# Optimization experiments

Hardware: AMD Instinct MI355X
Metric: run time of the kernel (lower is better)

Reference implementation:

```python
import jax, jax.numpy as jnp
import numpy as np

B, L, D, H = 2, 2048, 512, 8
DH = D // H
THRESHOLD = 0.1


def setup_inputs() -> dict:
    key = jax.random.key(0)
    ks = jax.random.split(key, 8)
    s = 0.02  # weight scale to keep activations sane
    return {
        "q_x": jax.random.normal(ks[0], (B, L, D), jnp.float32),
        "k_x": jax.random.normal(ks[1], (B, L, D), jnp.float32),
        "v_x": jax.random.normal(ks[2], (B, L, D), jnp.float32),
        "energy_coeffs": jax.random.normal(ks[3], (B, L, 16), jnp.float32),
        "Wq": jax.random.normal(ks[4], (D, D), jnp.float32) * s,
        "bq": jnp.zeros((D,), jnp.float32),
        "Wk": jax.random.normal(ks[5], (D, D), jnp.float32) * s,
        "bk": jnp.zeros((D,), jnp.float32),
        "Wv": jax.random.normal(ks[6], (D, D), jnp.float32) * s,
        "bv": jnp.zeros((D,), jnp.float32),
        "Wo": jax.random.normal(ks[7], (D, D), jnp.float32) * s,
        "bo": jnp.zeros((D,), jnp.float32),
    }


def reference(q_x, k_x, v_x, energy_coeffs, Wq, bq, Wk, bk, Wv, bv, Wo, bo):
    b, l, d = q_x.shape
    # QKV projections (torch Linear: x @ W.T + b), split heads -> [B,H,L,Dh]
    Q = (q_x @ Wq.T + bq).reshape(b, l, H, DH).transpose(0, 2, 1, 3)
    K = (k_x @ Wk.T + bk).reshape(b, -1, H, DH).transpose(0, 2, 1, 3)
    V = (v_x @ Wv.T + bv).reshape(b, -1, H, DH).transpose(0, 2, 1, 3)
    scores = jnp.einsum("bhqd,bhkd->bhqk", Q, K) / jnp.sqrt(jnp.float32(DH))
    # straight-through energy-based key mask
    energy = jnp.abs(energy_coeffs).mean(axis=-1)  # [B, Lk]
    soft = jax.nn.sigmoid((energy - THRESHOLD) * 10.0)
    hard = (energy > THRESHOLD).astype(q_x.dtype)
    mask_val = soft + jax.lax.stop_gradient(hard - soft)  # fwd=hard, grad=soft
    scores = scores + (1.0 - mask_val)[:, None, None, :] * (-1e9)
    attn = jax.nn.softmax(scores, axis=-1)
    out = jnp.einsum("bhqk,bhkd->bhqd", attn, V)
    out = out.transpose(0, 2, 1, 3).reshape(b, l, d)
    return out @ Wo.T + bo
```

## Files before the change

### kernel.cpp

```cpp
#include <hip/hip_runtime.h>
#include <stdint.h>

#define B_ 2
#define L_ 2048
#define D_ 512
#define H_ 8
#define DH_ 64

using frag8 = __attribute__((ext_vector_type(8))) short;
using bf4   = __attribute__((ext_vector_type(4))) short;
using f32x4 = __attribute__((ext_vector_type(4))) float;
using u32x4 = __attribute__((ext_vector_type(4))) unsigned int;

#define QSC 0.18033688011112042f

__device__ __forceinline__ unsigned short f2bf(float f) {
    unsigned int u = __float_as_uint(f);
    u += 0x7fffu + ((u >> 16) & 1u);
    return (unsigned short)(u >> 16);
}

__device__ __forceinline__ unsigned int cvtpk(float lo, float hi_) {
    unsigned int r;
    asm("v_cvt_pk_bf16_f32 %0, %1, %2" : "=v"(r) : "v"(lo), "v"(hi_));
    return r;
}

__device__ __forceinline__ void gl2lds16(const void* g, void* lds) {
    __builtin_amdgcn_global_load_lds((const __attribute__((address_space(1))) void*)g,
                                     (__attribute__((address_space(3))) void*)lds,
                                     16, 0, 0);
}

template<int N>
__device__ __forceinline__ void vmwait() {
    asm volatile("s_waitcnt vmcnt(%0)" :: "n"(N) : "memory");
}

__global__ __launch_bounds__(256) void cvt_mask_kernel(
    const float* __restrict__ qx, const float* __restrict__ kx, const float* __restrict__ vx,
    const float* __restrict__ Wq, const float* __restrict__ Wk, const float* __restrict__ Wv,
    const float* __restrict__ Wo, const float* __restrict__ ec,
    unsigned short* qb, unsigned short* kb, unsigned short* vb,
    unsigned short* wqb, unsigned short* wkb, unsigned short* wvb, unsigned short* wob,
    float* __restrict__ mk)
{
    const long NA = (long)B_ * L_ * D_;
    const long NW = (long)D_ * D_;
    const long total4 = (3 * NA + 4 * NW) / 4;
    long q4 = (long)blockIdx.x * 256 + threadIdx.x;
    if (q4 < total4) {
        long i = q4 * 4;
        const float* src; unsigned short* dst; long off;
        if (i < NA)            { src = qx; dst = qb; off = i; }
        else if (i < 2 * NA)   { src = kx; dst = kb; off = i - NA; }
        else if (i < 3 * NA)   { src = vx; dst = vb; off = i - 2 * NA; }
        else {
            long j = i - 3 * NA;
            int w = (int)(j / NW);
            off = j - (long)w * NW;
            src = (w == 0) ? Wq : (w == 1) ? Wk : (w == 2) ? Wv : Wo;
            dst = (w == 0) ? wqb : (w == 1) ? wkb : (w == 2) ? wvb : wob;
        }
        float4 v = *(const float4*)(src + off);
        ushort4 o;
        o.x = f2bf(v.x); o.y = f2bf(v.y); o.z = f2bf(v.z); o.w = f2bf(v.w);
        *(ushort4*)(dst + off) = o;
    } else {
        long i = q4 - total4;
        if (i < B_ * L_) {
            const float4* p4 = (const float4*)(ec + i * 16);
            float s = 0.0f;
#pragma unroll
            for (int j = 0; j < 4; ++j) {
                float4 v = p4[j];
                s += fabsf(v.x) + fabsf(v.y) + fabsf(v.z) + fabsf(v.w);
            }
            float energy = s * (1.0f / 16.0f);
            mk[i] = (energy > 0.1f) ? 0.0f : -1.0e9f;
        }
    }
}

struct GemmArgs { const unsigned short* A; const unsigned short* W;
                  const float* bias; void* C; int mode; };

template<int BM, int BN>
__global__ __launch_bounds__(256) void gemm_kernel(GemmArgs a0, GemmArgs a1, GemmArgs a2,
                                                   int M, int N, int K)
{
    const int nwg = gridDim.x * gridDim.y * gridDim.z;
    int flat = blockIdx.x + gridDim.x * (blockIdx.y + gridDim.y * blockIdx.z);
    int swz  = (flat & 7) * (nwg >> 3) + (flat >> 3);
    const int bx = swz % gridDim.x;
    int t2 = swz / gridDim.x;
    const int by = t2 % gridDim.y;
    const int bz = t2 / gridDim.y;

    GemmArgs ga = bz == 0 ? a0 : (bz == 1 ? a1 : a2);
    const unsigned short* __restrict__ A = ga.A;
    const unsigned short* __restrict__ W = ga.W;
    const float* __restrict__ bias = ga.bias;

    constexpr int MF = BM / 32;
    constexpr int NF = BN / 32;
    constexpr int NL = BM / 32 + BN / 32;

    __shared__ __align__(16) unsigned short As[2][BM * 64];
    __shared__ __align__(16) unsigned short Bs[2][BN * 64];

    const int tid  = threadIdx.x;
    const int lane = tid & 63;
    const int wave = tid >> 6;
    const int hi   = lane >> 4;
    const int ln   = lane & 15;
    const int wr   = wave >> 1;
    const int wc   = wave & 1;

    const long mBase = (long)by * BM;
    const long nBase = (long)bx * BN;

    f32x4 acc[MF][NF];
#pragma unroll
    for (int m = 0; m < MF; ++m)
#pragma unroll
        for (int n = 0; n < NF; ++n) acc[m][n] = (f32x4){0.f, 0.f, 0.f, 0.f};

#define GSTAGE(KT, BUF) do {                                                    \
    _Pragma("unroll")                                                           \
    for (int i_ = 0; i_ < BM / 32; ++i_) {                                      \
        int cl_ = i_ * 256 + tid;                                               \
        int r_ = cl_ >> 3, c_ = cl_ & 7, s_ = c_ ^ (r_ & 7);                    \
        gl2lds16(A + (mBase + r_) * K + (KT) + s_ * 8, As[BUF] + cl_ * 8);      \
    }                                                                           \
    _Pragma("unroll")                                                           \
    for (int i_ = 0; i_ < BN / 32; ++i_) {                                      \
        int cl_ = i_ * 256 + tid;                                               \
        int r_ = cl_ >> 3, c_ = cl_ & 7, s_ = c_ ^ (r_ & 7);                    \
        gl2lds16(W + (nBase + r_) * K + (KT) + s_ * 8, Bs[BUF] + cl_ * 8);      \
    }                                                                           \
} while (0)

    GSTAGE(0, 0);

    const int nk = K / 64;
    for (int t = 0; t < nk; ++t) {
        const int buf = t & 1;
        if (t + 1 < nk) {
            GSTAGE((t + 1) * 64, buf ^ 1);
            vmwait<NL>();
        } else {
            vmwait<0>();
        }
        __builtin_amdgcn_s_barrier();
        __builtin_amdgcn_sched_barrier(0);

        frag8 af[2][MF], bfr[2][NF];
#pragma unroll
        for (int kk = 0; kk < 2; ++kk) {
#pragma unroll
            for (int m = 0; m < MF; ++m) {
                int row = wr * (BM / 2) + m * 16 + ln;
                int c = (kk * 4 + hi) ^ (row & 7);
                af[kk][m] = *(const frag8*)(As[buf] + row * 64 + c * 8);
            }
#pragma unroll
            for (int n = 0; n < NF; ++n) {
                int row = wc * (BN / 2) + n * 16 + ln;
                int c = (kk * 4 + hi) ^ (row & 7);
                bfr[kk][n] = *(const frag8*)(Bs[buf] + row * 64 + c * 8);
            }
        }
        __builtin_amdgcn_s_setprio(1);
#pragma unroll
        for (int kk = 0; kk < 2; ++kk)
#pragma unroll
            for (int m = 0; m < MF; ++m)
#pragma unroll
                for (int n = 0; n < NF; ++n)
                    acc[m][n] = __builtin_amdgcn_mfma_f32_16x16x32_bf16(af[kk][m], bfr[kk][n], acc[m][n], 0, 0, 0);
        __builtin_amdgcn_s_setprio(0);
        __builtin_amdgcn_sched_barrier(0);
        __builtin_amdgcn_s_barrier();
    }
#undef GSTAGE

    const int mode = ga.mode;
#pragma unroll
    for (int m = 0; m < MF; ++m) {
#pragma unroll
        for (int n = 0; n < NF; ++n) {
            long col = nBase + wc * (BN / 2) + n * 16 + ln;
            float bv = bias[col];
#pragma unroll
            for (int j = 0; j < 4; ++j) {
                long row = mBase + wr * (BM / 2) + m * 16 + hi * 4 + j;
                float v = acc[m][n][j] + bv;
                if (mode == 3) {
                    ((float*)ga.C)[row * N + col] = v;
                } else if (mode == 2) {
                    int dh = (int)col & 63;
                    int swv = ((dh & 7) << 1) | ((dh >> 3) & 1);
                    long nt = (row & ~63L) | (long)(((((int)(row >> 2)) & 15) ^ swv) << 2) | (row & 3);
                    ((unsigned short*)ga.C)[col * (long)(B_ * L_) + nt] = f2bf(v);
                } else {
                    if (mode == 1) v *= QSC;
                    ((unsigned short*)ga.C)[row * N + col] = f2bf(v);
                }
            }
        }
    }
}

__global__ __launch_bounds__(512, 4) void attn_kernel(
    const unsigned short* __restrict__ Qg, const unsigned short* __restrict__ Kg,
    const unsigned short* __restrict__ Vt, const float* __restrict__ mkg,
    unsigned short* __restrict__ Og)
{
    const int tid  = threadIdx.x;
    const int lane = tid & 63;
    const int wave = tid >> 6;
    const int grp  = wave >> 2;
    const int wq   = wave & 3;
    const int gtid = tid & 255;
    const int hi   = lane >> 4;
    const int ln   = lane & 15;

    const int bh = blockIdx.y;
    const int b  = bh >> 3, h = bh & 7;
    const unsigned short* Qb = Qg + ((long)b * L_) * D_ + h * DH_;
    const unsigned short* Kb = Kg + ((long)b * L_) * D_ + h * DH_;
    const unsigned short* Vb = Vt + (long)(h * DH_) * (B_ * L_) + (long)b * L_;
    const float* mkb = mkg + (long)b * L_;

    __shared__ __align__(16) char smem[65536];
    unsigned short* KsG = (unsigned short*)(smem + grp * 32768);
    unsigned short* VsG = (unsigned short*)(smem + grp * 32768 + 16384);

    const int q0 = blockIdx.x * 64 + wq * 16;

    frag8 qf[2];
#pragma unroll
    for (int ks = 0; ks < 2; ++ks)
        qf[ks] = *(const frag8*)(Qb + (long)(q0 + ln) * D_ + ks * 32 + hi * 8);

    const int sw  = ((ln & 7) << 1) | ((ln >> 3) & 1);
    const int sl0 = ((hi     ) ^ sw) << 2;
    const int sl1 = ((hi + 4 ) ^ sw) << 2;
    const int sl2 = ((hi + 8 ) ^ sw) << 2;
    const int sl3 = ((hi + 12) ^ sw) << 2;

#define STAGE(TT, BUF) do {                                                     \
    _Pragma("unroll")                                                           \
    for (int c2_ = 0; c2_ < 2; ++c2_) {                                         \
        int cl_ = c2_ * 256 + gtid;                                             \
        int r_ = cl_ >> 3, c_ = cl_ & 7;                                        \
        gl2lds16(Kb + (long)((TT) * 64 + r_) * D_ + ((c_ ^ (r_ & 7)) << 3),     \
                 KsG + (BUF) * 4096 + cl_ * 8);                                 \
        gl2lds16(Vb + (long)r_ * (B_ * L_) + (TT) * 64 + (c_ << 3),             \
                 VsG + (BUF) * 4096 + cl_ * 8);                                 \
    }                                                                           \
} while (0)

    f32x4 o[4];
#pragma unroll
    for (int g = 0; g < 4; ++g) o[g] = (f32x4){0.f, 0.f, 0.f, 0.f};
    float m_run = -__builtin_inff();
    float l_run = 0.0f;
    float scp[16];

    auto SOFTPV = [&](const unsigned short* Vl) {
        float a0 = fmaxf(fmaxf(scp[0], scp[1]), scp[2]);
        float a1 = fmaxf(fmaxf(scp[3], scp[4]), scp[5]);
        float a2 = fmaxf(fmaxf(scp[6], scp[7]), scp[8]);
        float a3 = fmaxf(fmaxf(scp[9], scp[10]), scp[11]);
        float a4 = fmaxf(fmaxf(scp[12], scp[13]), scp[14]);
        float tl = fmaxf(fmaxf(fmaxf(a0, a1), a2), fmaxf(fmaxf(a3, a4), scp[15]));
        float tmax = fmaxf(tl, __shfl_xor(tl, 16));
        tmax = fmaxf(tmax, __shfl_xor(tmax, 32));

        if (!__all(tmax <= m_run + 8.0f)) {
            float m_new = fmaxf(m_run, tmax);
            float alpha = __builtin_amdgcn_exp2f(m_run - m_new);
            float b0 = __shfl(alpha, 4 * hi + 0);
            float b1 = __shfl(alpha, 4 * hi + 1);
            float b2 = __shfl(alpha, 4 * hi + 2);
            float b3 = __shfl(alpha, 4 * hi + 3);
#pragma unroll
            for (int g = 0; g < 4; ++g) {
                o[g][0] *= b0; o[g][1] *= b1; o[g][2] *= b2; o[g][3] *= b3;
            }
            l_run *= alpha;
            m_run = m_new;
        }

        float p[16];
#pragma unroll
        for (int j = 0; j < 16; ++j) p[j] = __builtin_amdgcn_exp2f(scp[j] - m_run);
        float s01 = (p[0] + p[1]) + (p[2] + p[3]);
        float s23 = (p[4] + p[5]) + (p[6] + p[7]);
        float s45 = (p[8] + p[9]) + (p[10] + p[11]);
        float s67 = (p[12] + p[13]) + (p[14] + p[15]);
        float ps = (s01 + s23) + (s45 + s67);
        ps += __shfl_xor(ps, 16);
        ps += __shfl_xor(ps, 32);
        l_run += ps;

        union PU { u32x4 u; frag8 f; } p0u, p1u;
        p0u.u = (u32x4){cvtpk(p[0], p[1]),  cvtpk(p[2], p[3]),
                        cvtpk(p[4], p[5]),  cvtpk(p[6], p[7])};
        p1u.u = (u32x4){cvtpk(p[8], p[9]),  cvtpk(p[10], p[11]),
                        cvtpk(p[12], p[13]), cvtpk(p[14], p[15])};

        __builtin_amdgcn_s_setprio(1);
#pragma unroll
        for (int g = 0; g < 4; ++g) {
            int rowb = (g * 16 + ln) * 64;
            bf4 v0 = *(const bf4*)(Vl + rowb + sl0);
            bf4 v1 = *(const bf4*)(Vl + rowb + sl1);
            bf4 v2 = *(const bf4*)(Vl + rowb + sl2);
            bf4 v3 = *(const bf4*)(Vl + rowb + sl3);
            frag8 vf0 = __builtin_shufflevector(v0, v1, 0, 1, 2, 3, 4, 5, 6, 7);
            frag8 vf1 = __builtin_shufflevector(v2, v3, 0, 1, 2, 3, 4, 5, 6, 7);
            o[g] = __builtin_amdgcn_mfma_f32_16x16x32_bf16(p0u.f, vf0, o[g], 0, 0, 0);
            o[g] = __builtin_amdgcn_mfma_f32_16x16x32_bf16(p1u.f, vf1, o[g], 0, 0, 0);
        }
        __builtin_amdgcn_s_setprio(0);
    };

    auto QKSAVE = [&](const unsigned short* Kl, int T) {
        float4 m40 = *(const float4*)(mkb + T * 64 +      4 * hi);
        float4 m41 = *(const float4*)(mkb + T * 64 + 16 + 4 * hi);
        float4 m42 = *(const float4*)(mkb + T * 64 + 32 + 4 * hi);
        float4 m43 = *(const float4*)(mkb + T * 64 + 48 + 4 * hi);
        f32x4 sv[4];
#pragma unroll
        for (int sh = 0; sh < 4; ++sh) sv[sh] = (f32x4){0.f, 0.f, 0.f, 0.f};
        __builtin_amdgcn_s_setprio(1);
#pragma unroll
        for (int sh = 0; sh < 4; ++sh) {
            int key = sh * 16 + ln;
#pragma unroll
            for (int ks = 0; ks < 2; ++ks) {
                frag8 kf = *(const frag8*)(Kl + key * 64 + (((ks * 4 + hi) ^ (ln & 7)) << 3));
                sv[sh] = __builtin_amdgcn_mfma_f32_16x16x32_bf16(kf, qf[ks], sv[sh], 0, 0, 0);
            }
        }
        __builtin_amdgcn_s_setprio(0);
        scp[0]  = sv[0][0] + m40.x; scp[1]  = sv[0][1] + m40.y;
        scp[2]  = sv[0][2] + m40.z; scp[3]  = sv[0][3] + m40.w;
        scp[4]  = sv[1][0] + m41.x; scp[5]  = sv[1][1] + m41.y;
        scp[6]  = sv[1][2] + m41.z; scp[7]  = sv[1][3] + m41.w;
        scp[8]  = sv[2][0] + m42.x; scp[9]  = sv[2][1] + m42.y;
        scp[10] = sv[2][2] + m42.z; scp[11] = sv[2][3] + m42.w;
        scp[12] = sv[3][0] + m43.x; scp[13] = sv[3][1] + m43.y;
        scp[14] = sv[3][2] + m43.z; scp[15] = sv[3][3] + m43.w;
    };

    STAGE(grp, 0);
    vmwait<0>();
    __builtin_amdgcn_s_barrier();
    __builtin_amdgcn_sched_barrier(0);
    STAGE(2 + grp, 1);
    QKSAVE(KsG, grp);

    for (int i = 1; i < 16; ++i) {
        const int buf = i & 1;
        SOFTPV(VsG + (buf ^ 1) * 4096);
        vmwait<0>();
        __builtin_amdgcn_s_barrier();
        __builtin_amdgcn_sched_barrier(0);
        if (i < 15) STAGE(2 * (i + 1) + grp, buf ^ 1);
        QKSAVE(KsG + buf * 4096, 2 * i + grp);
    }
    SOFTPV(VsG + 4096);
#undef STAGE

    __syncthreads();
    float* oX = (float*)smem;
    float* mX = (float*)(smem + 64 * 68 * 4);
    float* lX = mX + 64;

    if (grp == 1) {
#pragma unroll
        for (int g = 0; g < 4; ++g)
#pragma unroll
            for (int j = 0; j < 4; ++j)
                oX[(wq * 16 + 4 * hi + j) * 68 + g * 16 + ln] = o[g][j];
        if (hi == 0) { mX[wq * 16 + ln] = m_run; lX[wq * 16 + ln] = l_run; }
    }
    __syncthreads();
    if (grp == 0) {
#pragma unroll
        for (int j = 0; j < 4; ++j) {
            int q = 4 * hi + j;
            float mA = __shfl(m_run, q);
            float lA = __shfl(l_run, q);
            float mB = mX[wq * 16 + q];
            float lB = lX[wq * 16 + q];
            float mm = fmaxf(mA, mB);
            float aA = __builtin_amdgcn_exp2f(mA - mm);
            float aB = __builtin_amdgcn_exp2f(mB - mm);
            float inv = 1.0f / (lA * aA + lB * aB);
            aA *= inv; aB *= inv;
#pragma unroll
            for (int g = 0; g < 4; ++g) {
                float v = o[g][j] * aA + oX[(wq * 16 + q) * 68 + g * 16 + ln] * aB;
                long idx = ((long)b * L_ + q0 + q) * D_ + h * DH_ + g * 16 + ln;
                Og[idx] = f2bf(v);
            }
        }
    }
}

extern "C" void kernel_launch(void* const* d_in, const int* in_sizes, int n_in,
                              void* d_out, int out_size, void* d_ws, size_t ws_size,
                              hipStream_t stream)
{
    const float* qx = (const float*)d_in[0];
    const float* kx = (const float*)d_in[1];
    const float* vx = (const float*)d_in[2];
    const float* ec = (const float*)d_in[3];
    const float* Wq = (const float*)d_in[4];
    const float* bq = (const float*)d_in[5];
    const float* Wk = (const float*)d_in[6];
    const float* bk = (const float*)d_in[7];
    const float* Wv = (const float*)d_in[8];
    const float* bv = (const float*)d_in[9];
    const float* Wo = (const float*)d_in[10];
    const float* bo = (const float*)d_in[11];
    float* out = (float*)d_out;

    const long NA = (long)B_ * L_ * D_;
    const long NW = (long)D_ * D_;

    unsigned short* qb  = (unsigned short*)d_ws;
    unsigned short* kb  = qb + NA;
    unsigned short* vb  = kb + NA;
    unsigned short* wqb = vb + NA;
    unsigned short* wkb = wqb + NW;
    unsigned short* wvb = wkb + NW;
    unsigned short* wob = wvb + NW;
    unsigned short* Qp  = wob + NW;
    unsigned short* Kp  = Qp + NA;
    unsigned short* Vtp = Kp + NA;
    unsigned short* Ap  = qb;
    float*          mk  = (float*)(Vtp + NA);

    const long total4 = (3 * NA + 4 * NW) / 4;
    const long nblk = (total4 + B_ * L_ + 255) / 256;
    cvt_mask_kernel<<<dim3((unsigned)nblk), dim3(256), 0, stream>>>(
        qx, kx, vx, Wq, Wk, Wv, Wo, ec, qb, kb, vb, wqb, wkb, wvb, wob, mk);

    GemmArgs zq = {qb, wqb, bq, Qp, 1};
    GemmArgs zk = {kb, wkb, bk, Kp, 0};
    GemmArgs zv = {vb, wvb, bv, Vtp, 2};
    gemm_kernel<64, 128><<<dim3(4, 64, 3), dim3(256), 0, stream>>>(zq, zk, zv, B_ * L_, D_, D_);

    attn_kernel<<<dim3(L_ / 64, B_ * H_), dim3(512), 0, stream>>>(Qp, Kp, Vtp, mk, Ap);

    GemmArgs zo = {Ap, wob, bo, out, 3};
    gemm_kernel<64, 64><<<dim3(8, 64, 1), dim3(256), 0, stream>>>(zo, zo, zo, B_ * L_, D_, D_);
}
```

Baseline: 74.55 us.

## Prefetch mask, fold bias/mask into MFMA accumulators, shrink GEMM tiles

The attention kernel now loads the key-mask values for the next tile one iteration ahead and seeds the QK MFMA accumulators with them, so the separate add after the MFMA disappears. The cross-lane max and sum reductions use three independent shuffles instead of two dependent ones. In the GEMM the bias is preloaded into the accumulators. The QKV and output GEMMs use smaller tiles to launch more blocks, which adds occupancy at the cost of some data reuse and extra registers for the prefetched mask.

```diff
diff --git a/kernel.cpp b/kernel.cpp
--- a/kernel.cpp
+++ b/kernel.cpp
@@ -122,9 +122,11 @@
 
     f32x4 acc[MF][NF];
 #pragma unroll
-    for (int m = 0; m < MF; ++m)
-#pragma unroll
-        for (int n = 0; n < NF; ++n) acc[m][n] = (f32x4){0.f, 0.f, 0.f, 0.f};
+    for (int n = 0; n < NF; ++n) {
+        float bv = bias[nBase + wc * (BN / 2) + n * 16 + ln];
+#pragma unroll
+        for (int m = 0; m < MF; ++m) acc[m][n] = (f32x4){bv, bv, bv, bv};
+    }
 
 #define GSTAGE(KT, BUF) do {                                                    \
     _Pragma("unroll")                                                           \
@@ -191,11 +193,10 @@
 #pragma unroll
         for (int n = 0; n < NF; ++n) {
             long col = nBase + wc * (BN / 2) + n * 16 + ln;
-            float bv = bias[col];
 #pragma unroll
             for (int j = 0; j < 4; ++j) {
                 long row = mBase + wr * (BM / 2) + m * 16 + hi * 4 + j;
-                float v = acc[m][n][j] + bv;
+                float v = acc[m][n][j];
                 if (mode == 3) {
                     ((float*)ga.C)[row * N + col] = v;
                 } else if (mode == 2) {
@@ -262,22 +263,32 @@
     }                                                                           \
 } while (0)
 
+#define LOADM(TT, A0, A1, A2, A3) do {                                          \
+    A0 = *(const f32x4*)(mkb + (TT) * 64 +      4 * hi);                        \
+    A1 = *(const f32x4*)(mkb + (TT) * 64 + 16 + 4 * hi);                        \
+    A2 = *(const f32x4*)(mkb + (TT) * 64 + 32 + 4 * hi);                        \
+    A3 = *(const f32x4*)(mkb + (TT) * 64 + 48 + 4 * hi);                        \
+} while (0)
+
     f32x4 o[4];
 #pragma unroll
     for (int g = 0; g < 4; ++g) o[g] = (f32x4){0.f, 0.f, 0.f, 0.f};
     float m_run = -__builtin_inff();
     float l_run = 0.0f;
-    float scp[16];
+    f32x4 scp[4];
+    f32x4 mc0, mc1, mc2, mc3;
+    f32x4 mn0, mn1, mn2, mn3;
 
     auto SOFTPV = [&](const unsigned short* Vl) {
-        float a0 = fmaxf(fmaxf(scp[0], scp[1]), scp[2]);
-        float a1 = fmaxf(fmaxf(scp[3], scp[4]), scp[5]);
-        float a2 = fmaxf(fmaxf(scp[6], scp[7]), scp[8]);
-        float a3 = fmaxf(fmaxf(scp[9], scp[10]), scp[11]);
-        float a4 = fmaxf(fmaxf(scp[12], scp[13]), scp[14]);
-        float tl = fmaxf(fmaxf(fmaxf(a0, a1), a2), fmaxf(fmaxf(a3, a4), scp[15]));
-        float tmax = fmaxf(tl, __shfl_xor(tl, 16));
-        tmax = fmaxf(tmax, __shfl_xor(tmax, 32));
+        float a0 = fmaxf(fmaxf(scp[0][0], scp[0][1]), fmaxf(scp[0][2], scp[0][3]));
+        float a1 = fmaxf(fmaxf(scp[1][0], scp[1][1]), fmaxf(scp[1][2], scp[1][3]));
+        float a2 = fmaxf(fmaxf(scp[2][0], scp[2][1]), fmaxf(scp[2][2], scp[2][3]));
+        float a3 = fmaxf(fmaxf(scp[3][0], scp[3][1]), fmaxf(scp[3][2], scp[3][3]));
+        float tl = fmaxf(fmaxf(a0, a1), fmaxf(a2, a3));
+        float tA = __shfl_xor(tl, 16);
+        float tB = __shfl_xor(tl, 32);
+        float tC = __shfl_xor(tl, 48);
+        float tmax = fmaxf(fmaxf(tl, tA), fmaxf(tB, tC));
 
         if (!__all(tmax <= m_run + 8.0f)) {
             float m_new = fmaxf(m_run, tmax);
@@ -296,15 +307,19 @@
 
         float p[16];
 #pragma unroll
-        for (int j = 0; j < 16; ++j) p[j] = __builtin_amdgcn_exp2f(scp[j] - m_run);
+        for (int sh = 0; sh < 4; ++sh)
+#pragma unroll
+            for (int r = 0; r < 4; ++r)
+                p[sh * 4 + r] = __builtin_amdgcn_exp2f(scp[sh][r] - m_run);
         float s01 = (p[0] + p[1]) + (p[2] + p[3]);
         float s23 = (p[4] + p[5]) + (p[6] + p[7]);
         float s45 = (p[8] + p[9]) + (p[10] + p[11]);
         float s67 = (p[12] + p[13]) + (p[14] + p[15]);
         float ps = (s01 + s23) + (s45 + s67);
-        ps += __shfl_xor(ps, 16);
-        ps += __shfl_xor(ps, 32);
-        l_run += ps;
+        float pA = __shfl_xor(ps, 16);
+        float pB = __shfl_xor(ps, 32);
+        float pC = __shfl_xor(ps, 48);
+        l_run += (ps + pA) + (pB + pC);
 
         union PU { u32x4 u; frag8 f; } p0u, p1u;
         p0u.u = (u32x4){cvtpk(p[0], p[1]),  cvtpk(p[2], p[3]),
@@ -328,14 +343,8 @@
         __builtin_amdgcn_s_setprio(0);
     };
 
-    auto QKSAVE = [&](const unsigned short* Kl, int T) {
-        float4 m40 = *(const float4*)(mkb + T * 64 +      4 * hi);
-        float4 m41 = *(const float4*)(mkb + T * 64 + 16 + 4 * hi);
-        float4 m42 = *(const float4*)(mkb + T * 64 + 32 + 4 * hi);
-        float4 m43 = *(const float4*)(mkb + T * 64 + 48 + 4 * hi);
-        f32x4 sv[4];
-#pragma unroll
-        for (int sh = 0; sh < 4; ++sh) sv[sh] = (f32x4){0.f, 0.f, 0.f, 0.f};
+    auto QKSAVE = [&](const unsigned short* Kl) {
+        scp[0] = mc0; scp[1] = mc1; scp[2] = mc2; scp[3] = mc3;
         __builtin_amdgcn_s_setprio(1);
 #pragma unroll
         for (int sh = 0; sh < 4; ++sh) {
@@ -343,26 +352,20 @@
 #pragma unroll
             for (int ks = 0; ks < 2; ++ks) {
                 frag8 kf = *(const frag8*)(Kl + key * 64 + (((ks * 4 + hi) ^ (ln & 7)) << 3));
-                sv[sh] = __builtin_amdgcn_mfma_f32_16x16x32_bf16(kf, qf[ks], sv[sh], 0, 0, 0);
+                scp[sh] = __builtin_amdgcn_mfma_f32_16x16x32_bf16(kf, qf[ks], scp[sh], 0, 0, 0);
             }
         }
         __builtin_amdgcn_s_setprio(0);
-        scp[0]  = sv[0][0] + m40.x; scp[1]  = sv[0][1] + m40.y;
-        scp[2]  = sv[0][2] + m40.z; scp[3]  = sv[0][3] + m40.w;
-        scp[4]  = sv[1][0] + m41.x; scp[5]  = sv[1][1] + m41.y;
-        scp[6]  = sv[1][2] + m41.z; scp[7]  = sv[1][3] + m41.w;
-        scp[8]  = sv[2][0] + m42.x; scp[9]  = sv[2][1] + m42.y;
-        scp[10] = sv[2][2] + m42.z; scp[11] = sv[2][3] + m42.w;
-        scp[12] = sv[3][0] + m43.x; scp[13] = sv[3][1] + m43.y;
-        scp[14] = sv[3][2] + m43.z; scp[15] = sv[3][3] + m43.w;
     };
 
     STAGE(grp, 0);
+    LOADM(grp, mc0, mc1, mc2, mc3);
     vmwait<0>();
     __builtin_amdgcn_s_barrier();
     __builtin_amdgcn_sched_barrier(0);
     STAGE(2 + grp, 1);
-    QKSAVE(KsG, grp);
+    LOADM(2 + grp, mn0, mn1, mn2, mn3);
+    QKSAVE(KsG);
 
     for (int i = 1; i < 16; ++i) {
         const int buf = i & 1;
@@ -371,10 +374,13 @@
         __builtin_amdgcn_s_barrier();
         __builtin_amdgcn_sched_barrier(0);
         if (i < 15) STAGE(2 * (i + 1) + grp, buf ^ 1);
-        QKSAVE(KsG + buf * 4096, 2 * i + grp);
+        mc0 = mn0; mc1 = mn1; mc2 = mn2; mc3 = mn3;
+        if (i < 15) LOADM(2 * (i + 1) + grp, mn0, mn1, mn2, mn3);
+        QKSAVE(KsG + buf * 4096);
     }
     SOFTPV(VsG + 4096);
 #undef STAGE
+#undef LOADM
 
     __syncthreads();
     float* oX = (float*)smem;
@@ -455,10 +461,10 @@
     GemmArgs zq = {qb, wqb, bq, Qp, 1};
     GemmArgs zk = {kb, wkb, bk, Kp, 0};
     GemmArgs zv = {vb, wvb, bv, Vtp, 2};
-    gemm_kernel<64, 128><<<dim3(4, 64, 3), dim3(256), 0, stream>>>(zq, zk, zv, B_ * L_, D_, D_);
+    gemm_kernel<64, 64><<<dim3(8, 64, 3), dim3(256), 0, stream>>>(zq, zk, zv, B_ * L_, D_, D_);
 
     attn_kernel<<<dim3(L_ / 64, B_ * H_), dim3(512), 0, stream>>>(Qp, Kp, Vtp, mk, Ap);
 
     GemmArgs zo = {Ap, wob, bo, out, 3};
-    gemm_kernel<64, 64><<<dim3(8, 64, 1), dim3(256), 0, stream>>>(zo, zo, zo, B_ * L_, D_, D_);
-}
+    gemm_kernel<32, 64><<<dim3(8, 128, 1), dim3(256), 0, stream>>>(zo, zo, zo, B_ * L_, D_, D_);
+}
```

Result: no change. 74.34 us (-0.3%).
